# Kernel tuning notes

Hardware: AMD Instinct MI355X
Metric: run time of the kernel (lower is better)

The kernel has to match this reference:

```python
import jax, jax.numpy as jnp
import numpy as np

HEADS = 12
DIM_HEAD = 64
PATCHES = 196  # tokens_to_attend (space attention)
DIM = 768
BATCH = 8
FRAMES = 16
TOKENS = FRAMES * PATCHES + 1  # + CLS


def setup_inputs() -> dict:
    key = jax.random.key(0)
    k1, k2, k3 = jax.random.split(key, 3)
    x = jax.random.normal(k1, (BATCH, TOKENS, DIM), dtype=jnp.float32)
    # small init scale keeps softmax logits in a sane range
    W_qkv = jax.random.normal(k2, (DIM, 3 * HEADS * DIM_HEAD), dtype=jnp.float32) * 0.02
    W_0 = jax.random.normal(k3, (HEADS * DIM_HEAD, DIM), dtype=jnp.float32) * 0.02
    return {"x": x, "W_qkv": W_qkv, "W_0": W_0}


def _mhsa(q, k, v, scale):
    # q: [g,h,i,d], k/v: [g,h,j,d]
    s = jnp.einsum('ghid,ghjd->ghij', q, k) * scale
    a = jax.nn.softmax(s, axis=-1)
    return jnp.einsum('ghij,ghjd->ghid', a, v)


def reference(x, W_qkv, W_0):
    b, t, _ = x.shape
    h, dh, p = HEADS, DIM_HEAD, PATCHES
    scale = dh ** -0.5

    qkv = x @ W_qkv  # [b,t,dh*3*h], flattened in (d, k, h) order per einops pattern
    qkv = qkv.reshape(b, t, dh, 3, h)
    q = jnp.transpose(qkv[:, :, :, 0, :], (0, 3, 1, 2))  # [b,h,t,d]
    k = jnp.transpose(qkv[:, :, :, 1, :], (0, 3, 1, 2))
    v = jnp.transpose(qkv[:, :, :, 2, :], (0, 3, 1, 2))

    # CLS query attends over ALL space-time tokens
    cls_q, q3 = q[:, :, :1], q[:, :, 1:]
    out_cls = _mhsa(cls_q, k, v, scale)  # [b,h,1,d]

    cls_k, k3 = k[:, :, :1], k[:, :, 1:]
    cls_v, v3 = v[:, :, :1], v[:, :, 1:]

    f = (t - 1) // p  # frames

    def space_rearrange(z):  # 'b h (f p) d -> (b f) h p d'
        z = z.reshape(b, h, f, p, dh)
        return jnp.transpose(z, (0, 2, 1, 3, 4)).reshape(b * f, h, p, dh)

    q_sep = space_rearrange(q3)
    k_sep = space_rearrange(k3)
    v_sep = space_rearrange(v3)

    # broadcast CLS key/value to every frame group: 'b ... -> (b tile) ...'
    cls_k = jnp.repeat(cls_k, f, axis=0)  # [b*f,h,1,d]
    cls_v = jnp.repeat(cls_v, f, axis=0)

    kk = jnp.concatenate((cls_k, k_sep), axis=2)  # [b*f,h,p+1,d]
    vv = jnp.concatenate((cls_v, v_sep), axis=2)

    out_sp = _mhsa(q_sep, kk, vv, scale)  # [b*f,h,p,d]

    # merge: '(b f) h p d -> b h (f p) d' (space=True path)
    out_sp = out_sp.reshape(b, f, h, p, dh)
    out_sp = jnp.transpose(out_sp, (0, 2, 1, 3, 4)).reshape(b, h, f * p, dh)

    out = jnp.concatenate((out_cls, out_sp), axis=2)  # [b,h,t,d]
    out = jnp.transpose(out, (0, 2, 1, 3)).reshape(b, t, h * dh)
    return out @ W_0
```

## Files before the change

kernel.cpp:

```cpp
#include <hip/hip_runtime.h>
#include <hip/hip_bf16.h>
#include <cstdint>

typedef unsigned short u16;
typedef uint32_t u32;
typedef __attribute__((ext_vector_type(8))) u16 u16x8;
typedef __attribute__((ext_vector_type(4))) u16 u16x4;
typedef __attribute__((ext_vector_type(8))) __bf16 bf16x8;
typedef __attribute__((ext_vector_type(4))) float f32x4;

#define B_    8
#define T_    3137
#define H_    12
#define F_    16
#define D_    768
#define M1    25096
#define VSTR  3200
#define NSPL  8
#define SPK   400

__device__ __forceinline__ u16 f2bf(float f) {
  unsigned u = __float_as_uint(f);
  return (u16)((u + 0x7FFFu + ((u >> 16) & 1u)) >> 16);
}
__device__ __forceinline__ float b2f(u16 v) {
  return __uint_as_float(((unsigned)v) << 16);
}

#define GLL(g, l) __builtin_amdgcn_global_load_lds( \
    (const __attribute__((address_space(1))) void*)(g), \
    (__attribute__((address_space(3))) void*)(l), 16, 0, 0)

__device__ __forceinline__ void dsr(bf16x8& d, u32 abyte) {
  asm volatile("ds_read_b128 %0, %1" : "=v"(d) : "v"(abyte));
}

#define BARR  __builtin_amdgcn_s_barrier()
#define LGKM0 asm volatile("s_waitcnt lgkmcnt(0)")
#define SCB   __builtin_amdgcn_sched_barrier(0)
#define PRI1  __builtin_amdgcn_s_setprio(1)
#define PRI0  __builtin_amdgcn_s_setprio(0)

__global__ __launch_bounds__(256) void k_cvt_x(const float* __restrict__ x,
                                               u16* __restrict__ xb, int n4) {
  int i = blockIdx.x * 256 + threadIdx.x;
  if (i >= n4) return;
  float4 v = ((const float4*)x)[i];
  u16x4 o = { f2bf(v.x), f2bf(v.y), f2bf(v.z), f2bf(v.w) };
  *(u16x4*)(xb + (size_t)i * 4) = o;
}

__global__ __launch_bounds__(256) void k_transpose(const float* __restrict__ in,
                                                   u16* __restrict__ out,
                                                   int R, int C, int qkvperm) {
  __shared__ float tile[32][33];
  int c0 = blockIdx.x * 32, r0 = blockIdx.y * 32;
  int tx = threadIdx.x, ty = threadIdx.y;
  #pragma unroll
  for (int i = ty; i < 32; i += 8)
    tile[i][tx] = in[(size_t)(r0 + i) * C + c0 + tx];
  __syncthreads();
  #pragma unroll
  for (int i = ty; i < 32; i += 8) {
    int c = c0 + i;
    int orow;
    if (qkvperm) {
      int d = c / 36, rem = c - d * 36;
      int comp = rem / 12, hh = rem - comp * 12;
      orow = comp * 768 + hh * 64 + d;
    } else {
      orow = c;
    }
    out[(size_t)orow * R + r0 + tx] = f2bf(tile[tx][i]);
  }
}

template<int EPI, int NX>
__global__ __launch_bounds__(256, 2) void k_gemm(const u16* __restrict__ A,
                                                 const u16* __restrict__ Bm,
                                                 float* __restrict__ outF,
                                                 u16* __restrict__ Qb,
                                                 u16* __restrict__ Kb,
                                                 u16* __restrict__ Vt) {
  __shared__ u16 lds[32768];
  const int tid = threadIdx.x;
  const int lane = tid & 63;
  const int wid = tid >> 6;
  const int wr = wid >> 1, wc = wid & 1;
  const int li = lane & 15, lg = lane >> 4;

  const int nwg = NX * 197;
  const int q = nwg >> 3, r = nwg & 7;
  const int g = blockIdx.x;
  const int xcd = g & 7, pos = g >> 3;
  const int s = ((xcd < r) ? xcd * (q + 1) : r * (q + 1) + (xcd - r) * q) + pos;
  const int arow0 = (s / NX) * 128;
  const int brow0 = (s % NX) * 128;

  const int srow = wid * 32 + (lane >> 3);
  const int scol = ((lane & 7) ^ (lane >> 3)) * 8;
  const u16* gA = A  + (size_t)(arow0 + srow) * 768 + scol;
  const u16* gB = Bm + (size_t)(brow0 + srow) * 768 + scol;

  const u32 ldsb = (u32)(uintptr_t)(__attribute__((address_space(3))) u16*)(&lds[0]);
  const u32 e0 = (u32)((lg ^ (li & 7)) * 16);
  const u32 e1 = (u32)(((lg + 4) ^ (li & 7)) * 16);
  const u32 aA = ldsb + (u32)(wr * 64 + li) * 128;
  const u32 aB = ldsb + 16384 + (u32)(wc * 64 + li) * 128;

  f32x4 acc[4][4] = {};

#define STAGE(TB, KS) do { const int kb_ = (KS) * 64; \
    _Pragma("unroll") for (int c_ = 0; c_ < 4; ++c_) { \
      GLL(gA + kb_ + c_ * 8 * 768, lds + (TB) * 16384 + wid * 2048 + c_ * 512); \
      GLL(gB + kb_ + c_ * 8 * 768, lds + (TB) * 16384 + 8192 + wid * 2048 + c_ * 512); \
    } \
  } while (0)

#define STEP(CUR, KV) do { \
    { const int ks_ = ((KV) + 1 < 12) ? (KV) + 1 : 11; STAGE((CUR) ^ 1, ks_); } \
    asm volatile("s_waitcnt vmcnt(8)"); \
    BARR; \
    bf16x8 af[4][2], bfr[4][2]; \
    _Pragma("unroll") for (int m = 0; m < 4; ++m) { \
      dsr(af[m][0], aA + (CUR) * 32768 + m * 2048 + e0); \
      dsr(af[m][1], aA + (CUR) * 32768 + m * 2048 + e1); } \
    _Pragma("unroll") for (int n = 0; n < 4; ++n) { \
      dsr(bfr[n][0], aB + (CUR) * 32768 + n * 2048 + e0); \
      dsr(bfr[n][1], aB + (CUR) * 32768 + n * 2048 + e1); } \
    LGKM0; SCB; PRI1; \
    _Pragma("unroll") for (int m = 0; m < 4; ++m) \
    _Pragma("unroll") for (int n = 0; n < 4; ++n) { \
      acc[m][n] = __builtin_amdgcn_mfma_f32_16x16x32_bf16(af[m][0], bfr[n][0], acc[m][n], 0, 0, 0); \
      acc[m][n] = __builtin_amdgcn_mfma_f32_16x16x32_bf16(af[m][1], bfr[n][1], acc[m][n], 0, 0, 0); } \
    PRI0; BARR; \
  } while (0)

  STAGE(0, 0);

  #pragma unroll 1
  for (int kk = 0; kk < 12; kk += 2) {
    STEP(0, kk);
    STEP(1, kk + 1);
  }
#undef STAGE
#undef STEP

  if (EPI == 0) {
    #pragma unroll
    for (int m = 0; m < 4; ++m)
      #pragma unroll
      for (int n = 0; n < 4; ++n) {
        const int colp = brow0 + wc * 64 + n * 16 + li;
        #pragma unroll
        for (int rr = 0; rr < 4; ++rr) {
          const int row = arow0 + wr * 64 + m * 16 + lg * 4 + rr;
          if (row < M1)
            __builtin_nontemporal_store(acc[m][n][rr], outF + (size_t)row * 768 + colp);
        }
      }
  } else {
    const int comp = brow0 / 768;
    const int b0r = arow0 / T_;
    const int RB = (b0r + 1) * T_;
    __syncthreads();
    if (comp < 2) {
      u16* tl = &lds[0];
      #pragma unroll
      for (int m = 0; m < 4; ++m)
        #pragma unroll
        for (int n = 0; n < 4; ++n)
          #pragma unroll
          for (int rr = 0; rr < 4; ++rr)
            tl[(wr * 64 + m * 16 + lg * 4 + rr) * 136 + wc * 64 + n * 16 + li] =
                f2bf(acc[m][n][rr]);
      __syncthreads();
      u16* dst = (comp == 0) ? Qb : Kb;
      const int hh0 = (brow0 - comp * 768) >> 6;
      const int grp = tid >> 4, li2 = tid & 15;
      #pragma unroll
      for (int pass = 0; pass < 16; ++pass) {
        const int idx = pass * 16 + grp;
        const int row = idx >> 1, hl = idx & 1;
        const int rg = arow0 + row;
        if (rg >= M1) continue;
        const int bb = (rg >= RB) ? b0r + 1 : b0r;
        const int tt = rg - bb * T_;
        const size_t bh = (size_t)bb * H_ + hh0 + hl;
        *(u16x4*)(dst + ((bh * T_ + tt) << 6) + li2 * 4) =
            *(const u16x4*)(tl + row * 136 + hl * 64 + li2 * 4);
      }
    } else {
      u16* tl = &lds[0];
      #pragma unroll
      for (int m = 0; m < 4; ++m)
        #pragma unroll
        for (int n = 0; n < 4; ++n)
          #pragma unroll
          for (int rr = 0; rr < 4; ++rr)
            tl[(wr * 64 + m * 16 + lg * 4 + rr) * 130 + wc * 64 + n * 16 + li] =
                f2bf(acc[m][n][rr]);
      __syncthreads();
      const int vcol0 = brow0 - 1536;
      #pragma unroll 1
      for (int cc = 0; cc < 32; ++cc) {
        const int c = wid * 32 + cc;
        const int vcol = vcol0 + c;
        const int hh = vcol >> 6, dd = vcol & 63;
        #pragma unroll
        for (int half = 0; half < 2; ++half) {
          const int tloc = half * 64 + lane;
          const int rg = arow0 + tloc;
          if (rg >= M1) continue;
          const int bb = (rg >= RB) ? b0r + 1 : b0r;
          const int tt = rg - bb * T_;
          Vt[(((size_t)bb * H_ + hh) * 64 + dd) * VSTR + tt] = tl[tloc * 130 + c];
        }
      }
    }
  }
}

__global__ __launch_bounds__(512, 2) void k_attn_sp(const u16* __restrict__ Qb,
                                                    const u16* __restrict__ Kb,
                                                    const u16* __restrict__ Vt,
                                                    u16* __restrict__ AO) {
  __shared__ u16 Ks[224 * 64];
  __shared__ u16 Vs[4 * 64 * 64];
  __shared__ u16 P[8][16 * 232];
  const int bid = blockIdx.x;
  const int h = bid % H_;
  const int f = (bid / H_) % F_;
  const int b = bid / (H_ * F_);
  const int tid = threadIdx.x;
  const int lane = tid & 63, w = tid >> 6;
  const int li = lane & 15, lg = lane >> 4;
  const size_t bh = (size_t)b * H_ + h;
  const u16* Qp = Qb + bh * T_ * 64;
  const u16* Kp = Kb + bh * T_ * 64;
  const u16* Vp = Vt + bh * 64 * VSTR;
  u16* ps = &P[w][0];

  if (w < 7) {
    #pragma unroll
    for (int p = 0; p < 4; ++p) {
      const int c = (w * 4 + p) * 64 + lane;
      const int key = c >> 3, sp = lane & 7;
      const int tok = (key == 0) ? 0 : f * 196 + key;
      GLL(Kp + (size_t)tok * 64 + ((sp ^ (key & 7)) * 8), Ks + c * 8);
    }
  }
  {
    const int d = tid & 63, kg = (tid >> 6) & 3, sh = tid >> 8;
    #pragma unroll
    for (int st = 0; st < 2; ++st) {
      const int stt = sh + st * 2;
      const u16* src = Vp + (size_t)d * VSTR + f * 196 + stt * 64 + kg * 16;
      u16x4 a0 = *(const u16x4*)(src);
      u16x4 a1 = *(const u16x4*)(src + 4);
      u16x4 a2 = *(const u16x4*)(src + 8);
      u16x4 a3 = *(const u16x4*)(src + 12);
      if (stt == 0 && kg == 0) a0[0] = Vp[(size_t)d * VSTR];
      u16* row = Vs + stt * 4096 + d * 64;
      const int s0 = (kg * 2) ^ (d & 7), s1 = (kg * 2 + 1) ^ (d & 7);
      u16x8 w0 = { a0[0], a0[1], a0[2], a0[3], a1[0], a1[1], a1[2], a1[3] };
      u16x8 w1 = { a2[0], a2[1], a2[2], a2[3], a3[0], a3[1], a3[2], a3[3] };
      *(u16x8*)(row + s0 * 8) = w0;
      *(u16x8*)(row + s1 * 8) = w1;
    }
  }
  __syncthreads();

  for (int mt = w; mt < 13; mt += 8) {
    const int pp = mt * 16 + li;
    const int ppc = pp < 196 ? pp : 195;
    const size_t tq = 1 + f * 196 + ppc;
    const bf16x8 qf0 = *(const bf16x8*)(Qp + tq * 64 + lg * 8);
    const bf16x8 qf1 = *(const bf16x8*)(Qp + tq * 64 + 32 + lg * 8);

    f32x4 s[14] = {};
    #pragma unroll
    for (int n = 0; n < 14; ++n) {
      const int key = n * 16 + li;
      const u16* kp = Ks + key * 64;
      const bf16x8 kf0 = *(const bf16x8*)(kp + ((lg ^ (li & 7)) * 8));
      const bf16x8 kf1 = *(const bf16x8*)(kp + (((lg + 4) ^ (li & 7)) * 8));
      s[n] = __builtin_amdgcn_mfma_f32_16x16x32_bf16(qf0, kf0, s[n], 0, 0, 0);
      s[n] = __builtin_amdgcn_mfma_f32_16x16x32_bf16(qf1, kf1, s[n], 0, 0, 0);
    }

    float rsum[4];
    #pragma unroll
    for (int r = 0; r < 4; ++r) {
      float vals[14];
      float mx = -1e30f;
      #pragma unroll
      for (int n = 0; n < 14; ++n) {
        const int key = n * 16 + li;
        float sv = s[n][r] * 0.125f;
        vals[n] = (key < 197) ? sv : -1e30f;
        mx = fmaxf(mx, vals[n]);
      }
      #pragma unroll
      for (int msk = 1; msk < 16; msk <<= 1) mx = fmaxf(mx, __shfl_xor(mx, msk));
      float sum = 0.f;
      #pragma unroll
      for (int n = 0; n < 14; ++n) {
        const int key = n * 16 + li;
        float p = (key < 197) ? __expf(vals[n] - mx) : 0.f;
        sum += p;
        ps[(lg * 4 + r) * 232 + key] = f2bf(p);
      }
      #pragma unroll
      for (int msk = 1; msk < 16; msk <<= 1) sum += __shfl_xor(sum, msk);
      rsum[r] = sum;
    }

    f32x4 o[4] = {};
    #pragma unroll
    for (int ks = 0; ks < 7; ++ks) {
      const bf16x8 pf = *(const bf16x8*)(ps + li * 232 + ks * 32 + lg * 8);
      const int slot = ((ks & 1) * 4 + lg);
      #pragma unroll
      for (int n = 0; n < 4; ++n) {
        const int d = n * 16 + li;
        const bf16x8 vf = *(const bf16x8*)(Vs + (ks >> 1) * 4096 + d * 64 +
                                           ((slot ^ (li & 7)) * 8));
        o[n] = __builtin_amdgcn_mfma_f32_16x16x32_bf16(pf, vf, o[n], 0, 0, 0);
      }
    }

    #pragma unroll
    for (int n = 0; n < 4; ++n)
      #pragma unroll
      for (int r = 0; r < 4; ++r)
        ps[(lg * 4 + r) * 64 + n * 16 + li] = f2bf(o[n][r] / rsum[r]);
    #pragma unroll
    for (int p2 = 0; p2 < 2; ++p2) {
      const int row = p2 * 8 + (lane >> 3);
      const int ch = lane & 7;
      const int ppo = mt * 16 + row;
      if (ppo < 196) {
        const size_t t = 1 + (size_t)f * 196 + ppo;
        *(u16x8*)(AO + ((size_t)b * T_ + t) * 768 + h * 64 + ch * 8) =
            *(const u16x8*)(ps + row * 64 + ch * 8);
      }
    }
  }
}

__global__ __launch_bounds__(256) void k_attn_cls1(const u16* __restrict__ Qb,
                                                   const u16* __restrict__ Kb,
                                                   const u16* __restrict__ Vt,
                                                   float* __restrict__ Pc) {
  __shared__ float qs[64];
  __shared__ float sv[SPK];
  __shared__ float red[8];
  const int bid = blockIdx.x;
  const int s = bid & (NSPL - 1);
  const int bh = bid >> 3;
  const u16* Qp = Qb + (size_t)bh * T_ * 64;
  const u16* Kp = Kb + (size_t)bh * T_ * 64;
  const u16* Vp = Vt + (size_t)bh * 64 * VSTR;
  const int base = s * SPK;
  const int nk = (T_ - base < SPK) ? (T_ - base) : SPK;
  const int tid = threadIdx.x;
  const int lane = tid & 63, w = tid >> 6;

  if (tid < 64) qs[tid] = b2f(Qp[tid]);
  for (int jj = nk + tid; jj < SPK; jj += 256) sv[jj] = 0.f;
  __syncthreads();

  float lmax = -1e30f;
  for (int jj = tid; jj < nk; jj += 256) {
    const u16* kp = Kp + (size_t)(base + jj) * 64;
    float acc = 0.f;
    #pragma unroll
    for (int d0 = 0; d0 < 64; d0 += 8) {
      u16x8 kv = *(const u16x8*)(kp + d0);
      #pragma unroll
      for (int e = 0; e < 8; ++e) acc += qs[d0 + e] * b2f(kv[e]);
    }
    acc *= 0.125f;
    sv[jj] = acc;
    lmax = fmaxf(lmax, acc);
  }
  #pragma unroll
  for (int msk = 32; msk; msk >>= 1) lmax = fmaxf(lmax, __shfl_xor(lmax, msk));
  if (lane == 0) red[w] = lmax;
  __syncthreads();
  const float bmax = fmaxf(fmaxf(red[0], red[1]), fmaxf(red[2], red[3]));

  float lsum = 0.f;
  for (int jj = tid; jj < nk; jj += 256) {
    float p = __expf(sv[jj] - bmax);
    sv[jj] = p;
    lsum += p;
  }
  #pragma unroll
  for (int msk = 32; msk; msk >>= 1) lsum += __shfl_xor(lsum, msk);
  if (lane == 0) red[4 + w] = lsum;
  __syncthreads();
  const float bsum = red[4] + red[5] + red[6] + red[7];

  const int d = tid >> 2, q4 = tid & 3;
  const u16* vp = Vp + (size_t)d * VSTR + base + q4 * (SPK / 4);
  const float* sp = &sv[q4 * (SPK / 4)];
  float o = 0.f;
  #pragma unroll
  for (int k4 = 0; k4 < SPK / 4; k4 += 4) {
    u16x4 vv = *(const u16x4*)(vp + k4);
    o += sp[k4]     * b2f(vv[0]) + sp[k4 + 1] * b2f(vv[1])
       + sp[k4 + 2] * b2f(vv[2]) + sp[k4 + 3] * b2f(vv[3]);
  }
  o += __shfl_xor(o, 1);
  o += __shfl_xor(o, 2);

  float* P = Pc + ((size_t)bh * NSPL + s) * 66;
  if (tid == 0) { P[0] = bmax; P[1] = bsum; }
  if (q4 == 0) P[2 + d] = o;
}

__global__ __launch_bounds__(64) void k_attn_cls2(const float* __restrict__ Pc,
                                                  u16* __restrict__ AO) {
  const int bh = blockIdx.x;
  const int d = threadIdx.x;
  const float* P = Pc + (size_t)bh * NSPL * 66;
  float m = -1e30f;
  #pragma unroll
  for (int s = 0; s < NSPL; ++s) m = fmaxf(m, P[s * 66]);
  float l = 0.f, o = 0.f;
  #pragma unroll
  for (int s = 0; s < NSPL; ++s) {
    const float wgt = __expf(P[s * 66] - m);
    l += wgt * P[s * 66 + 1];
    o += wgt * P[s * 66 + 2 + d];
  }
  const int b = bh / H_, h = bh - b * H_;
  AO[(size_t)b * T_ * 768 + h * 64 + d] = f2bf(o / l);
}

extern "C" void kernel_launch(void* const* d_in, const int* in_sizes, int n_in,
                              void* d_out, int out_size, void* d_ws, size_t ws_size,
                              hipStream_t stream) {
  const float* x    = (const float*)d_in[0];
  const float* Wqkv = (const float*)d_in[1];
  const float* W0   = (const float*)d_in[2];
  float* out = (float*)d_out;
  char* ws = (char*)d_ws;

  u16* xb    = (u16*)(ws);
  u16* wqkvT = (u16*)(ws + 38731776);
  u16* w0T   = (u16*)(ws + 42270720);
  u16* Qb    = (u16*)(ws + 43450368);
  u16* Kb    = (u16*)(ws + 81997824);
  u16* Vt    = (u16*)(ws + 120545280);
  u16* AO = xb;
  float* Pc = (float*)wqkvT;

  k_cvt_x<<<dim3(18822), dim3(256), 0, stream>>>(x, xb, (M1 * D_) / 4);
  k_transpose<<<dim3(72, 24), dim3(32, 8), 0, stream>>>(Wqkv, wqkvT, 768, 2304, 1);
  k_transpose<<<dim3(24, 24), dim3(32, 8), 0, stream>>>(W0, w0T, 768, 768, 0);
  k_gemm<1, 18><<<dim3(18 * 197), dim3(256), 0, stream>>>(xb, wqkvT, nullptr, Qb, Kb, Vt);
  k_attn_sp<<<dim3(1536), dim3(512), 0, stream>>>(Qb, Kb, Vt, AO);
  k_attn_cls1<<<dim3(96 * NSPL), dim3(256), 0, stream>>>(Qb, Kb, Vt, Pc);
  k_attn_cls2<<<dim3(96), dim3(64), 0, stream>>>(Pc, AO);
  k_gemm<0, 6><<<dim3(6 * 197), dim3(256), 0, stream>>>(AO, w0T, out, nullptr, nullptr, nullptr);
}
```

Before: 286.5 us.

## Load GEMM B operand directly to registers and fold softmax scale into Q

```diff
diff --git a/kernel.cpp b/kernel.cpp
--- a/kernel.cpp
+++ b/kernel.cpp
@@ -76,13 +76,13 @@
 }
 
 template<int EPI, int NX>
-__global__ __launch_bounds__(256, 2) void k_gemm(const u16* __restrict__ A,
+__global__ __launch_bounds__(256, 3) void k_gemm(const u16* __restrict__ A,
                                                  const u16* __restrict__ Bm,
                                                  float* __restrict__ outF,
                                                  u16* __restrict__ Qb,
                                                  u16* __restrict__ Kb,
                                                  u16* __restrict__ Vt) {
-  __shared__ u16 lds[32768];
+  __shared__ u16 lds[17408];
   const int tid = threadIdx.x;
   const int lane = tid & 63;
   const int wid = tid >> 6;
@@ -99,51 +99,59 @@
 
   const int srow = wid * 32 + (lane >> 3);
   const int scol = ((lane & 7) ^ (lane >> 3)) * 8;
-  const u16* gA = A  + (size_t)(arow0 + srow) * 768 + scol;
-  const u16* gB = Bm + (size_t)(brow0 + srow) * 768 + scol;
+  const u16* gA = A + (size_t)(arow0 + srow) * 768 + scol;
+
+  const u16* gBl = Bm + (size_t)(brow0 + wc * 64 + li) * 768 + lg * 8;
 
   const u32 ldsb = (u32)(uintptr_t)(__attribute__((address_space(3))) u16*)(&lds[0]);
   const u32 e0 = (u32)((lg ^ (li & 7)) * 16);
   const u32 e1 = (u32)(((lg + 4) ^ (li & 7)) * 16);
   const u32 aA = ldsb + (u32)(wr * 64 + li) * 128;
-  const u32 aB = ldsb + 16384 + (u32)(wc * 64 + li) * 128;
 
   f32x4 acc[4][4] = {};
-
-#define STAGE(TB, KS) do { const int kb_ = (KS) * 64; \
-    _Pragma("unroll") for (int c_ = 0; c_ < 4; ++c_) { \
-      GLL(gA + kb_ + c_ * 8 * 768, lds + (TB) * 16384 + wid * 2048 + c_ * 512); \
-      GLL(gB + kb_ + c_ * 8 * 768, lds + (TB) * 16384 + 8192 + wid * 2048 + c_ * 512); \
-    } \
+  bf16x8 bfr[4][2];
+
+#define STAGE_A(TB, KS) do { const int kb_ = (KS) * 64; \
+    _Pragma("unroll") for (int c_ = 0; c_ < 4; ++c_) \
+      GLL(gA + kb_ + c_ * 8 * 768, lds + (TB) * 8192 + wid * 2048 + c_ * 512); \
   } while (0)
 
+#define LOADB(KS) do { const int kb_ = (KS) * 64; \
+    _Pragma("unroll") for (int n_ = 0; n_ < 4; ++n_) \
+    _Pragma("unroll") for (int h_ = 0; h_ < 2; ++h_) \
+      bfr[n_][h_] = *(const bf16x8*)(gBl + n_ * 16 * 768 + kb_ + h_ * 32); \
+  } while (0)
+
 #define STEP(CUR, KV) do { \
-    { const int ks_ = ((KV) + 1 < 12) ? (KV) + 1 : 11; STAGE((CUR) ^ 1, ks_); } \
     asm volatile("s_waitcnt vmcnt(8)"); \
     BARR; \
-    bf16x8 af[4][2], bfr[4][2]; \
+    bf16x8 af[4][2]; \
     _Pragma("unroll") for (int m = 0; m < 4; ++m) { \
-      dsr(af[m][0], aA + (CUR) * 32768 + m * 2048 + e0); \
-      dsr(af[m][1], aA + (CUR) * 32768 + m * 2048 + e1); } \
-    _Pragma("unroll") for (int n = 0; n < 4; ++n) { \
-      dsr(bfr[n][0], aB + (CUR) * 32768 + n * 2048 + e0); \
-      dsr(bfr[n][1], aB + (CUR) * 32768 + n * 2048 + e1); } \
+      dsr(af[m][0], aA + (CUR) * 16384 + m * 2048 + e0); \
+      dsr(af[m][1], aA + (CUR) * 16384 + m * 2048 + e1); } \
+    { const int ks_ = ((KV) + 1 < 12) ? (KV) + 1 : 11; STAGE_A((CUR) ^ 1, ks_); } \
+    SCB; \
     LGKM0; SCB; PRI1; \
     _Pragma("unroll") for (int m = 0; m < 4; ++m) \
     _Pragma("unroll") for (int n = 0; n < 4; ++n) { \
       acc[m][n] = __builtin_amdgcn_mfma_f32_16x16x32_bf16(af[m][0], bfr[n][0], acc[m][n], 0, 0, 0); \
       acc[m][n] = __builtin_amdgcn_mfma_f32_16x16x32_bf16(af[m][1], bfr[n][1], acc[m][n], 0, 0, 0); } \
-    PRI0; BARR; \
+    PRI0; SCB; \
+    { const int kn_ = ((KV) + 1 < 12) ? (KV) + 1 : 11; LOADB(kn_); } \
+    SCB; \
+    BARR; \
   } while (0)
 
-  STAGE(0, 0);
+  STAGE_A(0, 0);
+  LOADB(0);
 
   #pragma unroll 1
   for (int kk = 0; kk < 12; kk += 2) {
     STEP(0, kk);
     STEP(1, kk + 1);
   }
-#undef STAGE
+#undef STAGE_A
+#undef LOADB
 #undef STEP
 
   if (EPI == 0) {
@@ -161,6 +169,7 @@
       }
   } else {
     const int comp = brow0 / 768;
+    const float qsc = (comp == 0) ? 0.125f : 1.0f;
     const int b0r = arow0 / T_;
     const int RB = (b0r + 1) * T_;
     __syncthreads();
@@ -173,7 +182,7 @@
           #pragma unroll
           for (int rr = 0; rr < 4; ++rr)
             tl[(wr * 64 + m * 16 + lg * 4 + rr) * 136 + wc * 64 + n * 16 + li] =
-                f2bf(acc[m][n][rr]);
+                f2bf(acc[m][n][rr] * qsc);
       __syncthreads();
       u16* dst = (comp == 0) ? Qb : Kb;
       const int hh0 = (brow0 - comp * 768) >> 6;
@@ -297,8 +306,7 @@
       #pragma unroll
       for (int n = 0; n < 14; ++n) {
         const int key = n * 16 + li;
-        float sv = s[n][r] * 0.125f;
-        vals[n] = (key < 197) ? sv : -1e30f;
+        vals[n] = (key < 197) ? s[n][r] : -1e30f;
         mx = fmaxf(mx, vals[n]);
       }
       #pragma unroll
@@ -381,7 +389,6 @@
       #pragma unroll
       for (int e = 0; e < 8; ++e) acc += qs[d0 + e] * b2f(kv[e]);
     }
-    acc *= 0.125f;
     sv[jj] = acc;
     lmax = fmaxf(lmax, acc);
   }
```

New measurement: 398.2 us. 1.39x slower.
